# Kernel tuning notes

Hardware: AMD Instinct MI355X
Metric: run time of the kernel (lower is better)

The kernel has to match this reference:

```python
import jax, jax.numpy as jnp
import numpy as np

IMG = 1024
STRIDES = [8, 16, 32, 64, 128]
SIZES = [32, 64, 128, 256, 512]
RATIOS = [0.5, 1.0, 2.0]
MIN_T = 0.4  # config.min_iou_thresh
MAX_T = 0.5  # config.max_iou_thresh (focal loss_type)
B, G = 32, 20  # batch, GT boxes per image (lengths = [20]*32)


def _make_anchors():
    """generate_anchors + get_anchor_shifts: centered anchors on each level's grid."""
    levels = []
    for stride, size in zip(STRIDES, SIZES):
        ws = np.array([size / np.sqrt(r) for r in RATIOS])
        hs = np.array([size * np.sqrt(r) for r in RATIOS])
        base = np.stack([-ws / 2, -hs / 2, ws / 2, hs / 2], axis=1)  # [3,4]
        g = IMG // stride
        xs = (np.arange(g) + 0.5) * stride
        sy, sx = np.meshgrid(xs, xs, indexing='ij')
        shifts = np.stack([sx, sy, sx, sy], axis=-1).reshape(-1, 1, 4)
        levels.append((shifts + base[None]).reshape(-1, 4).astype(np.float32))
    return levels


def setup_inputs() -> dict:
    key = jax.random.key(0)
    k1, k2, k3 = jax.random.split(key, 3)
    ctr = jax.random.uniform(k1, (B, G, 2), minval=64.0, maxval=float(IMG - 64))
    wh = jax.random.uniform(k2, (B, G, 2), minval=16.0, maxval=256.0)
    bb_coord = jnp.concatenate([ctr - 0.5 * wh, ctr + 0.5 * wh], axis=-1)  # [B,G,4] x1y1x2y2
    bird_ids = jax.random.randint(k3, (B, G), 1, 51, dtype=jnp.int32)
    anchors = _make_anchors()
    inp = {'bb_coord': bb_coord, 'bird_ids': bird_ids}
    for i, a in enumerate(anchors):
        inp[f'anchors_l{i}'] = jnp.asarray(a)
    return inp


def _iou(anch, gt):
    a = anch[None, :, None, :]
    g = gt[:, None, :, :]
    iw = jnp.clip(jnp.minimum(a[..., 2], g[..., 2]) - jnp.maximum(a[..., 0], g[..., 0]) + 1.0, 0.0)
    ih = jnp.clip(jnp.minimum(a[..., 3], g[..., 3]) - jnp.maximum(a[..., 1], g[..., 1]) + 1.0, 0.0)
    area_a = (anch[:, 2] - anch[:, 0] + 1.0) * (anch[:, 3] - anch[:, 1] + 1.0)  # [A]
    area_g = (gt[..., 2] - gt[..., 0] + 1.0) * (gt[..., 3] - gt[..., 1] + 1.0)  # [B,G]
    inter = iw * ih
    return inter / (area_a[None, :, None] + area_g[:, None, :] - inter)


def _bbox_transform(ex, gt):
    # ex [A,4] anchors, gt [B,A,4] assigned boxes -> [B,A,4] (dx,dy,dw,dh)
    ew = ex[:, 2] - ex[:, 0] + 1.0
    eh = ex[:, 3] - ex[:, 1] + 1.0
    ecx = ex[:, 0] + 0.5 * ew
    ecy = ex[:, 1] + 0.5 * eh
    gw = gt[..., 2] - gt[..., 0] + 1.0
    gh = gt[..., 3] - gt[..., 1] + 1.0
    gcx = gt[..., 0] + 0.5 * gw
    gcy = gt[..., 1] + 0.5 * gh
    return jnp.stack([(gcx - ecx) / ew, (gcy - ecy) / eh,
                      jnp.log(gw / ew), jnp.log(gh / eh)], axis=-1)


def _assign(bb_coord, bird_ids_f, anchors_list):
    n_lvl = len(anchors_list)
    max_ovs, argmaxs, gt_maxs, gt_args = [], [], [], []
    for anch in anchors_list:
        ov = _iou(anch, bb_coord)                 # [B,A,G]
        max_ovs.append(ov.max(axis=2))            # [B,A]
        argmaxs.append(ov.argmax(axis=2))         # [B,A]
        gt_maxs.append(ov.max(axis=1))            # [B,G]
        gt_args.append(ov.argmax(axis=1))         # [B,G]
    gt_max_level = jnp.stack(gt_maxs, axis=0).argmax(axis=0)  # [B,G]

    labels_out, reg_out = [], []
    brow = jnp.arange(B)[:, None]
    for lvl, anch in enumerate(anchors_list):
        A = anch.shape[0]
        max_ov, amax = max_ovs[lvl], argmaxs[lvl]
        assigned_box = bb_coord[brow, amax]        # [B,A,4]
        assigned_ids = bird_ids_f[brow, amax]      # [B,A]
        # force each GT's best anchor (on its best level) positive
        is_max = gt_max_level == lvl               # [B,G]
        safe_idx = jnp.where(is_max, gt_args[lvl], A)  # OOB -> dropped
        assigned_box = assigned_box.at[brow, safe_idx].set(bb_coord, mode='drop')
        assigned_ids = assigned_ids.at[brow, safe_idx].set(bird_ids_f, mode='drop')
        ignore = (max_ov >= MIN_T) & (max_ov < MAX_T)
        pos = max_ov >= MAX_T
        pos = pos.at[brow, safe_idx].set(True, mode='drop')
        labels = jnp.where(pos, assigned_ids, jnp.where(ignore, -1.0, 0.0))
        reg = jnp.where(pos[..., None], _bbox_transform(anch, assigned_box), 0.0)
        labels_out.append(labels.astype(jnp.int32))
        reg_out.append(reg)
    return jnp.concatenate(labels_out, axis=1), jnp.concatenate(reg_out, axis=1)


def reference(bb_coord, bird_ids, anchors_l0, anchors_l1, anchors_l2, anchors_l3, anchors_l4):
    anchors = [anchors_l0, anchors_l1, anchors_l2, anchors_l3, anchors_l4]
    labels, reg = _assign(bb_coord, bird_ids.astype(jnp.float32), anchors)
    return labels, reg
```

## Files before the change

kernel.cpp:

```cpp
#include <hip/hip_runtime.h>
#include <hip/hip_bf16.h>

#define NB 32
#define NG 20
#define A_TOTAL 65472
#define LAB_OFF ((size_t)NB * A_TOTAL)
#define NSLOT (NB * NG * 5)
#define KBIAS 0xC000000000000000ull

__device__ __forceinline__ float b2f(unsigned short u) {
    __hip_bfloat16 h;
    __builtin_memcpy(&h, &u, 2);
    return __bfloat162float(h);
}

__device__ __forceinline__ float4 ldbox(const void* p, int idx, int isbf) {
    if (isbf) {
        const unsigned short* q = (const unsigned short*)p + (size_t)idx * 4;
        return make_float4(b2f(q[0]), b2f(q[1]), b2f(q[2]), b2f(q[3]));
    }
    return ((const float4*)p)[idx];
}

__device__ __forceinline__ int detect_bf(const void* an0) {
    const unsigned short* u = (const unsigned short*)an0;
    return (fabsf(b2f(u[0]) + 18.6274f) < 0.5f &&
            fabsf(b2f(u[2]) - 26.6274f) < 0.5f) ? 1 : 0;
}

__device__ __forceinline__ float decode_id(const void* idsv, int i) {
    unsigned w = ((const unsigned*)idsv)[i];
    return (w <= 50u) ? (float)(int)w : __uint_as_float(w);
}

__device__ __forceinline__ float area1(float4 A) {
#pragma clang fp contract(off)
    return (A.z - A.x + 1.0f) * (A.w - A.y + 1.0f);
}

__device__ __forceinline__ void reg_transform(float4 A, float g0, float g1,
                                              float g2, float g3,
                                              float& t0, float& t1,
                                              float& t2, float& t3) {
#pragma clang fp contract(off)
    const float ew = A.z - A.x + 1.0f, eh = A.w - A.y + 1.0f;
    const float ecx = A.x + 0.5f * ew, ecy = A.y + 0.5f * eh;
    const float gw = g2 - g0 + 1.0f, gh = g3 - g1 + 1.0f;
    const float gcx = g0 + 0.5f * gw, gcy = g1 + 0.5f * gh;
    t0 = (gcx - ecx) / ew;
    t1 = (gcy - ecy) / eh;
    t2 = logf(gw / ew);
    t3 = logf(gh / eh);
}

__device__ __forceinline__ float iou32h(float4 A, float aa,
                                        float4 G, float ag) {
#pragma clang fp contract(off)
    float iw = fminf(A.z, G.z) - fmaxf(A.x, G.x) + 1.0f;
    iw = fmaxf(iw, 0.0f);
    float ih = fminf(A.w, G.w) - fmaxf(A.y, G.y) + 1.0f;
    ih = fmaxf(ih, 0.0f);
    float inter = iw * ih;
    float v = 0.0f;
    if (inter > 0.0f) v = inter / (aa + ag - inter);
    return v;
}

__global__ __launch_bounds__(256)
void kCodes(const void* __restrict__ bb, const void* __restrict__ idsv,
            const void* __restrict__ an0, const void* __restrict__ an1,
            const void* __restrict__ an2, const void* __restrict__ an3,
            const void* __restrict__ an4,
            float* __restrict__ out,
            unsigned long long* __restrict__ slots)
{
    __shared__ float4 sbox4[NG];
    __shared__ float  sag[NG];
    __shared__ float  sid[NG];
    __shared__ unsigned long long swk[NG][4];
    __shared__ float  swb[4][4];
    __shared__ int    sskip[NG];

    const int tid = threadIdx.x;
    const int b = blockIdx.y;
    const int c = blockIdx.x;
    const int isbf = detect_bf(an0);

    if (tid < NG) {
        const float4 G = ldbox(bb, b * NG + tid, isbf);
        sbox4[tid] = G;
        sag[tid] = area1(G);
        sid[tid] = decode_id(idsv, b * NG + tid);
    }

    int l, lbase, count, goff;
    if (c < 48)      { l = 0; lbase = c * 1024;        count = 1024; goff = 0; }
    else if (c < 60) { l = 1; lbase = (c - 48) * 1024; count = 1024; goff = 49152; }
    else if (c < 63) { l = 2; lbase = (c - 60) * 1024; count = 1024; goff = 61440; }
    else if (c == 63){ l = 3; lbase = 0;               count = 768;  goff = 64512; }
    else             { l = 4; lbase = 0;               count = 192;  goff = 65280; }
    const void* an = (l == 0) ? an0 : (l == 1) ? an1
                   : (l == 2) ? an2 : (l == 3) ? an3 : an4;

    float4 A[4];
    float aa[4];
    bool val[4];
#pragma unroll
    for (int k = 0; k < 4; ++k) {
        const int i = tid + k * 256;
        val[k] = (i < count);
        A[k] = val[k] ? ldbox(an, lbase + i, isbf)
                      : make_float4(1e8f, 1e8f, -1e8f, -1e8f);
        aa[k] = area1(A[k]);
    }

    {
        float mnx = fminf(fminf(A[0].x, A[1].x), fminf(A[2].x, A[3].x));
        float mny = fminf(fminf(A[0].y, A[1].y), fminf(A[2].y, A[3].y));
        float mxz = fmaxf(fmaxf(A[0].z, A[1].z), fmaxf(A[2].z, A[3].z));
        float mxw = fmaxf(fmaxf(A[0].w, A[1].w), fmaxf(A[2].w, A[3].w));
        for (int o = 32; o > 0; o >>= 1) {
            mnx = fminf(mnx, __shfl_xor(mnx, o));
            mny = fminf(mny, __shfl_xor(mny, o));
            mxz = fmaxf(mxz, __shfl_xor(mxz, o));
            mxw = fmaxf(mxw, __shfl_xor(mxw, o));
        }
        if ((tid & 63) == 0) {
            swb[tid >> 6][0] = mnx; swb[tid >> 6][1] = mny;
            swb[tid >> 6][2] = mxz; swb[tid >> 6][3] = mxw;
        }
    }
    __syncthreads();
    if (tid < NG) {
        const float bminx = fminf(fminf(swb[0][0], swb[1][0]), fminf(swb[2][0], swb[3][0]));
        const float bminy = fminf(fminf(swb[0][1], swb[1][1]), fminf(swb[2][1], swb[3][1]));
        const float bmaxz = fmaxf(fmaxf(swb[0][2], swb[1][2]), fmaxf(swb[2][2], swb[3][2]));
        const float bmaxw = fmaxf(fmaxf(swb[0][3], swb[1][3]), fmaxf(swb[2][3], swb[3][3]));
        const float4 G = sbox4[tid];
        sskip[tid] = (G.z - bminx + 1.0f <= 0.0f) ||
                     (bmaxz - G.x + 1.0f <= 0.0f) ||
                     (G.w - bminy + 1.0f <= 0.0f) ||
                     (bmaxw - G.y + 1.0f <= 0.0f);
    }
    __syncthreads();

    float mx[4] = {0.f, 0.f, 0.f, 0.f};
    int mg[4] = {0, 0, 0, 0};
    const int lane = tid & 63;
    const int wave = tid >> 6;
    const int base_idx = goff + lbase + tid;

    for (int g = 0; g < NG; ++g) {
        if (sskip[g]) {
            if (lane == 0) swk[g][wave] = 0ull;
            continue;
        }
        const float4 G = sbox4[g];
        const float ag = sag[g];
        float bvv = -1.0f;
        int bii = 0;
#pragma unroll
        for (int k = 0; k < 4; ++k) {
            const float v = iou32h(A[k], aa[k], G, ag);
            if (v > mx[k]) { mx[k] = v; mg[k] = g; }
            if (v > bvv)   { bvv = v; bii = base_idx + k * 256; }
        }
        if (__any(bvv > 0.0f)) {
            unsigned long long key = KBIAS
                | ((unsigned long long)__float_as_uint(bvv) << 32)
                | (unsigned)(~(unsigned)bii);
            for (int o = 32; o > 0; o >>= 1) {
                const unsigned long long ok = __shfl_xor(key, o);
                if (ok > key) key = ok;
            }
            if (lane == 0) swk[g][wave] = key;
        } else {
            if (lane == 0) swk[g][wave] = 0ull;
        }
    }

    float* lab = out + (size_t)b * A_TOTAL;
    float4* rp = (float4*)(out + LAB_OFF) + (size_t)b * A_TOTAL;
#pragma unroll
    for (int k = 0; k < 4; ++k) {
        if (!val[k]) continue;
        const int ga = base_idx + k * 256;
        const bool pos = (mx[k] >= 0.5f);
        lab[ga] = pos ? sid[mg[k]] : ((mx[k] >= 0.4f) ? -1.0f : 0.0f);
        float t0 = 0.f, t1 = 0.f, t2 = 0.f, t3 = 0.f;
        if (pos) {
            const float4 G = sbox4[mg[k]];
            reg_transform(A[k], G.x, G.y, G.z, G.w, t0, t1, t2, t3);
        }
        rp[ga] = make_float4(t0, t1, t2, t3);
    }

    __syncthreads();
    if (tid < NG) {
        unsigned long long k0 = swk[tid][0];
        for (int w = 1; w < 4; ++w)
            if (swk[tid][w] > k0) k0 = swk[tid][w];
        if (k0 != 0ull)
            atomicMax(&slots[(b * NG + tid) * 5 + l], k0);
    }
}

__global__ __launch_bounds__(64)
void kForce(const void* __restrict__ bb, const void* __restrict__ idsv,
            const void* __restrict__ an0, const void* __restrict__ an1,
            const void* __restrict__ an2, const void* __restrict__ an3,
            const void* __restrict__ an4,
            const unsigned long long* __restrict__ slots,
            float* __restrict__ out)
{
    __shared__ int sforce[NG];
    const int b = blockIdx.x;
    const int g = threadIdx.x;
    const int isbf = detect_bf(an0);

    if (g < NG) {
        const unsigned long long* s = &slots[(b * NG + g) * 5];
        unsigned long long best = 0ull;
        for (int l = 0; l < 5; ++l) {
            const unsigned long long v = s[l];
            const unsigned hi = (unsigned)(v >> 32);
            if (hi >= 0xC0000000u && hi > (unsigned)(best >> 32)) best = v;
        }
        sforce[g] = (best == 0ull) ? -1 : (int)(~(unsigned)best);
    }
    __syncthreads();

    if (g < NG) {
        const int a = sforce[g];
        if (a >= 0) {
            bool win = true;
            for (int g2 = g + 1; g2 < NG; ++g2)
                if (sforce[g2] == a) win = false;
            if (win) {
                int l, off;
                if (a < 49152)      { l = 0; off = 0; }
                else if (a < 61440) { l = 1; off = 49152; }
                else if (a < 64512) { l = 2; off = 61440; }
                else if (a < 65280) { l = 3; off = 64512; }
                else                { l = 4; off = 65280; }
                const void* an = (l == 0) ? an0 : (l == 1) ? an1
                               : (l == 2) ? an2 : (l == 3) ? an3 : an4;
                const float4 A = ldbox(an, a - off, isbf);
                const float4 G = ldbox(bb, b * NG + g, isbf);
                out[(size_t)b * A_TOTAL + a] = decode_id(idsv, b * NG + g);
                float t0, t1, t2, t3;
                reg_transform(A, G.x, G.y, G.z, G.w, t0, t1, t2, t3);
                ((float4*)(out + LAB_OFF))[(size_t)b * A_TOTAL + a]
                    = make_float4(t0, t1, t2, t3);
            }
        }
    }
}

__global__ __launch_bounds__(1024)
void kFused(const void* __restrict__ bb, const void* __restrict__ idsv,
            const void* __restrict__ an0, const void* __restrict__ an1,
            const void* __restrict__ an2, const void* __restrict__ an3,
            const void* __restrict__ an4,
            float* __restrict__ out)
{
    __shared__ float4 sbox4[NG];
    __shared__ float swv[NG][16];
    __shared__ int   swi[NG][16];
    __shared__ float lvv[NG][5];
    __shared__ int   lvi[NG][5];
    __shared__ float sid[NG];
    __shared__ int   sforce[NG];

    const int tid = threadIdx.x;
    const int b = blockIdx.x;
    const int isbf = detect_bf(an0);

    if (tid < NG) {
        sbox4[tid] = ldbox(bb, b * NG + tid, isbf);
        sid[tid] = decode_id(idsv, b * NG + tid);
    }
    __syncthreads();

    const void* ans[5] = {an0, an1, an2, an3, an4};
    const int lcount[5] = {49152, 12288, 3072, 768, 192};
    const int loffs[5]  = {0, 49152, 61440, 64512, 65280};
    const int lane = tid & 63;
    const int wave = tid >> 6;
    float* myCodes = out + (size_t)b * A_TOTAL;

    for (int l = 0; l < 5; ++l) {
        float bv[NG];
        int bi[NG];
#pragma unroll
        for (int g = 0; g < NG; ++g) { bv[g] = -1.0f; bi[g] = 0x7fffffff; }
        for (int i = tid; i < lcount[l]; i += 1024) {
            const float4 A = ldbox(ans[l], i, isbf);
            const float aa = area1(A);
            float mxv = -1.0f;
            int mgv = 0;
#pragma unroll
            for (int g = 0; g < NG; ++g) {
                const float4 G = sbox4[g];
                const float ag = area1(G);
                float v = iou32h(A, aa, G, ag);
                if (v > mxv) { mxv = v; mgv = g; }
                if (v > bv[g]) { bv[g] = v; bi[g] = i; }
            }
            const int cls = (mxv >= 0.5f) ? 2 : (mxv >= 0.4f) ? 1 : 0;
            myCodes[loffs[l] + i] = (float)(mgv | (cls << 5));
        }
#pragma unroll
        for (int g = 0; g < NG; ++g) {
            float v = bv[g];
            int ix = bi[g];
            for (int o = 32; o > 0; o >>= 1) {
                float ov = __shfl_xor(v, o);
                int   oi = __shfl_xor(ix, o);
                if (ov > v || (ov == v && oi < ix)) { v = ov; ix = oi; }
            }
            if (lane == 0) { swv[g][wave] = v; swi[g][wave] = ix; }
        }
        __syncthreads();
        if (tid < NG) {
            float v = swv[tid][0];
            int ix = swi[tid][0];
            for (int w = 1; w < 16; ++w) {
                float ov = swv[tid][w];
                int   oi = swi[tid][w];
                if (ov > v || (ov == v && oi < ix)) { v = ov; ix = oi; }
            }
            lvv[tid][l] = v;
            lvi[tid][l] = ix;
        }
        __syncthreads();
    }
    if (tid < NG) {
        int bl = 0;
#pragma unroll
        for (int l = 1; l < 5; ++l)
            if (lvv[tid][l] > lvv[tid][bl]) bl = l;
        sforce[tid] = loffs[bl] + lvi[tid][bl];
    }
    __syncthreads();

    float4* rp = (float4*)(out + LAB_OFF);
    for (int a = tid; a < A_TOTAL; a += 1024) {
        int l, off;
        if (a < 49152)      { l = 0; off = 0; }
        else if (a < 61440) { l = 1; off = 49152; }
        else if (a < 64512) { l = 2; off = 61440; }
        else if (a < 65280) { l = 3; off = 64512; }
        else                { l = 4; off = 65280; }
        const int code = (int)myCodes[a];
        const int mgv = code & 31;
        const int cls = code >> 5;
        int fg = -1;
#pragma unroll
        for (int g = 0; g < NG; ++g)
            if (sforce[g] == a) fg = g;
        const bool pos = (cls == 2) || (fg >= 0);
        const int ug = (fg >= 0) ? fg : mgv;
        myCodes[a] = pos ? sid[ug] : ((cls == 1) ? -1.0f : 0.0f);
        float t0 = 0.f, t1 = 0.f, t2 = 0.f, t3 = 0.f;
        if (pos) {
            const float4 A = ldbox(ans[l], a - off, isbf);
            const float4 G = sbox4[ug];
            reg_transform(A, G.x, G.y, G.z, G.w, t0, t1, t2, t3);
        }
        rp[(size_t)b * A_TOTAL + a] = make_float4(t0, t1, t2, t3);
    }
}

extern "C" void kernel_launch(void* const* d_in, const int* in_sizes, int n_in,
                              void* d_out, int out_size, void* d_ws, size_t ws_size,
                              hipStream_t stream) {
    const void* bb = d_in[0];
    const void* ids = d_in[1];
    const void* an[5] = {d_in[2], d_in[3], d_in[4], d_in[5], d_in[6]};
    if (n_in == 7) {
        for (int i = 0; i < 7; ++i) {
            switch (in_sizes[i]) {
                case 2560:   bb    = d_in[i]; break;
                case 640:    ids   = d_in[i]; break;
                case 196608: an[0] = d_in[i]; break;
                case 49152:  an[1] = d_in[i]; break;
                case 12288:  an[2] = d_in[i]; break;
                case 3072:   an[3] = d_in[i]; break;
                case 768:    an[4] = d_in[i]; break;
                default: break;
            }
        }
    }
    float* out = (float*)d_out;
    const size_t need = (size_t)NSLOT * sizeof(unsigned long long);

    if (ws_size >= need) {
        unsigned long long* slots = (unsigned long long*)d_ws;
        hipLaunchKernelGGL(kCodes, dim3(65, NB), dim3(256), 0, stream,
                           bb, ids, an[0], an[1], an[2], an[3], an[4],
                           out, slots);
        hipLaunchKernelGGL(kForce, dim3(NB), dim3(64), 0, stream,
                           bb, ids, an[0], an[1], an[2], an[3], an[4],
                           slots, out);
    } else {
        hipLaunchKernelGGL(kFused, dim3(NB), dim3(1024), 0, stream,
                           bb, ids, an[0], an[1], an[2], an[3], an[4], out);
    }
}
```

Measured before the change: 105.2 us.

## Assign contiguous anchors per thread with per-wave culling and vectorized label stores

Each thread now handles four consecutive anchors instead of four anchors spaced 256 apart. This lets the label output go out as one float4 store, and each wave covers a compact spatial region. The per-GT overlap cull now uses each wave's own anchor bounding box, computed with shuffles, rather than the whole block's box. That drops the shared-memory skip table and one block barrier, and lets more wave/GT pairs be skipped. In exchange, the per-anchor float4 loads and regression stores are strided across lanes, which can reduce coalescing. Tie-breaking indices and the culling decision are now computed per wave.

```diff
diff --git a/kernel.cpp b/kernel.cpp
--- a/kernel.cpp
+++ b/kernel.cpp
@@ -78,8 +78,6 @@
     __shared__ float  sag[NG];
     __shared__ float  sid[NG];
     __shared__ unsigned long long swk[NG][4];
-    __shared__ float  swb[4][4];
-    __shared__ int    sskip[NG];
 
     const int tid = threadIdx.x;
     const int b = blockIdx.y;
@@ -102,45 +100,27 @@
     const void* an = (l == 0) ? an0 : (l == 1) ? an1
                    : (l == 2) ? an2 : (l == 3) ? an3 : an4;
 
+    const int i0 = 4 * tid;
+    const bool valid = (i0 < count);
     float4 A[4];
     float aa[4];
-    bool val[4];
 #pragma unroll
     for (int k = 0; k < 4; ++k) {
-        const int i = tid + k * 256;
-        val[k] = (i < count);
-        A[k] = val[k] ? ldbox(an, lbase + i, isbf)
-                      : make_float4(1e8f, 1e8f, -1e8f, -1e8f);
+        A[k] = valid ? ldbox(an, lbase + i0 + k, isbf)
+                     : make_float4(1e8f, 1e8f, -1e8f, -1e8f);
         aa[k] = area1(A[k]);
     }
-
-    {
-        float mnx = fminf(fminf(A[0].x, A[1].x), fminf(A[2].x, A[3].x));
-        float mny = fminf(fminf(A[0].y, A[1].y), fminf(A[2].y, A[3].y));
-        float mxz = fmaxf(fmaxf(A[0].z, A[1].z), fmaxf(A[2].z, A[3].z));
-        float mxw = fmaxf(fmaxf(A[0].w, A[1].w), fmaxf(A[2].w, A[3].w));
-        for (int o = 32; o > 0; o >>= 1) {
-            mnx = fminf(mnx, __shfl_xor(mnx, o));
-            mny = fminf(mny, __shfl_xor(mny, o));
-            mxz = fmaxf(mxz, __shfl_xor(mxz, o));
-            mxw = fmaxf(mxw, __shfl_xor(mxw, o));
-        }
-        if ((tid & 63) == 0) {
-            swb[tid >> 6][0] = mnx; swb[tid >> 6][1] = mny;
-            swb[tid >> 6][2] = mxz; swb[tid >> 6][3] = mxw;
-        }
-    }
-    __syncthreads();
-    if (tid < NG) {
-        const float bminx = fminf(fminf(swb[0][0], swb[1][0]), fminf(swb[2][0], swb[3][0]));
-        const float bminy = fminf(fminf(swb[0][1], swb[1][1]), fminf(swb[2][1], swb[3][1]));
-        const float bmaxz = fmaxf(fmaxf(swb[0][2], swb[1][2]), fmaxf(swb[2][2], swb[3][2]));
-        const float bmaxw = fmaxf(fmaxf(swb[0][3], swb[1][3]), fmaxf(swb[2][3], swb[3][3]));
-        const float4 G = sbox4[tid];
-        sskip[tid] = (G.z - bminx + 1.0f <= 0.0f) ||
-                     (bmaxz - G.x + 1.0f <= 0.0f) ||
-                     (G.w - bminy + 1.0f <= 0.0f) ||
-                     (bmaxw - G.y + 1.0f <= 0.0f);
+    const int ga0 = goff + lbase + i0;
+
+    float wmnx = fminf(fminf(A[0].x, A[1].x), fminf(A[2].x, A[3].x));
+    float wmny = fminf(fminf(A[0].y, A[1].y), fminf(A[2].y, A[3].y));
+    float wmxz = fmaxf(fmaxf(A[0].z, A[1].z), fmaxf(A[2].z, A[3].z));
+    float wmxw = fmaxf(fmaxf(A[0].w, A[1].w), fmaxf(A[2].w, A[3].w));
+    for (int o = 32; o > 0; o >>= 1) {
+        wmnx = fminf(wmnx, __shfl_xor(wmnx, o));
+        wmny = fminf(wmny, __shfl_xor(wmny, o));
+        wmxz = fmaxf(wmxz, __shfl_xor(wmxz, o));
+        wmxw = fmaxf(wmxw, __shfl_xor(wmxw, o));
     }
     __syncthreads();
 
@@ -148,14 +128,17 @@
     int mg[4] = {0, 0, 0, 0};
     const int lane = tid & 63;
     const int wave = tid >> 6;
-    const int base_idx = goff + lbase + tid;
 
     for (int g = 0; g < NG; ++g) {
-        if (sskip[g]) {
+        const float4 G = sbox4[g];
+        const bool skip = (G.z - wmnx + 1.0f <= 0.0f) ||
+                          (wmxz - G.x + 1.0f <= 0.0f) ||
+                          (G.w - wmny + 1.0f <= 0.0f) ||
+                          (wmxw - G.y + 1.0f <= 0.0f);
+        if (skip) {
             if (lane == 0) swk[g][wave] = 0ull;
             continue;
         }
-        const float4 G = sbox4[g];
         const float ag = sag[g];
         float bvv = -1.0f;
         int bii = 0;
@@ -163,7 +146,7 @@
         for (int k = 0; k < 4; ++k) {
             const float v = iou32h(A[k], aa[k], G, ag);
             if (v > mx[k]) { mx[k] = v; mg[k] = g; }
-            if (v > bvv)   { bvv = v; bii = base_idx + k * 256; }
+            if (v > bvv)   { bvv = v; bii = ga0 + k; }
         }
         if (__any(bvv > 0.0f)) {
             unsigned long long key = KBIAS
@@ -179,20 +162,22 @@
         }
     }
 
-    float* lab = out + (size_t)b * A_TOTAL;
-    float4* rp = (float4*)(out + LAB_OFF) + (size_t)b * A_TOTAL;
-#pragma unroll
-    for (int k = 0; k < 4; ++k) {
-        if (!val[k]) continue;
-        const int ga = base_idx + k * 256;
-        const bool pos = (mx[k] >= 0.5f);
-        lab[ga] = pos ? sid[mg[k]] : ((mx[k] >= 0.4f) ? -1.0f : 0.0f);
-        float t0 = 0.f, t1 = 0.f, t2 = 0.f, t3 = 0.f;
-        if (pos) {
-            const float4 G = sbox4[mg[k]];
-            reg_transform(A[k], G.x, G.y, G.z, G.w, t0, t1, t2, t3);
-        }
-        rp[ga] = make_float4(t0, t1, t2, t3);
+    if (valid) {
+        float4 lv;
+        float* lvp = (float*)&lv;
+        float4* rp = (float4*)(out + LAB_OFF) + (size_t)b * A_TOTAL;
+#pragma unroll
+        for (int k = 0; k < 4; ++k) {
+            const bool pos = (mx[k] >= 0.5f);
+            lvp[k] = pos ? sid[mg[k]] : ((mx[k] >= 0.4f) ? -1.0f : 0.0f);
+            float t0 = 0.f, t1 = 0.f, t2 = 0.f, t3 = 0.f;
+            if (pos) {
+                const float4 G = sbox4[mg[k]];
+                reg_transform(A[k], G.x, G.y, G.z, G.w, t0, t1, t2, t3);
+            }
+            rp[ga0 + k] = make_float4(t0, t1, t2, t3);
+        }
+        *(float4*)(out + (size_t)b * A_TOTAL + ga0) = lv;
     }
 
     __syncthreads();
```

New measurement: 113.0 us. 1.07x slower.
